# Performance work log

Measured on AMD Instinct MI355X. Metric: run time of the kernel, lower is better.

The kernel has to match this reference:

```python
import jax, jax.numpy as jnp
import numpy as np

N_HEAD = 32
N_KV_HEAD = 8
HEAD_DIM = 64
ROPE_BASE = 10000.0


def _rope_cos_sin(T, dtype):
    # inv_freq over even dims; freqs: [T, HEAD_DIM//2]
    inv_freq = 1.0 / (ROPE_BASE ** (jnp.arange(0, HEAD_DIM, 2, dtype=jnp.float32) / HEAD_DIM))
    freqs = jnp.arange(T, dtype=jnp.float32)[:, None] * inv_freq[None, :]
    return jnp.cos(freqs).astype(dtype), jnp.sin(freqs).astype(dtype)


def _apply_rope(x, cos, sin):
    # x: [B, H, T, D]; cos/sin: [T, D//2]. Original chunks cat(freqs,freqs) so
    # cos1==cos2==cos(freqs), sin1==sin2==sin(freqs) -> standard rotate-half.
    x1, x2 = jnp.split(x, 2, axis=-1)
    c = cos[None, None]
    s = sin[None, None]
    return jnp.concatenate([x1 * c - x2 * s, x1 * s + x2 * c], axis=-1)


def setup_inputs() -> dict:
    key = jax.random.key(0)
    ks = jax.random.split(key, 5)
    B, T, C = 2, 2048, 2048
    kv_dim = N_KV_HEAD * HEAD_DIM
    sc = 1.0 / np.sqrt(C)
    return {
        "x": jax.random.normal(ks[0], (B, T, C), jnp.float32),
        "Wq": jax.random.normal(ks[1], (C, C), jnp.float32) * sc,
        "Wk": jax.random.normal(ks[2], (C, kv_dim), jnp.float32) * sc,
        "Wv": jax.random.normal(ks[3], (C, kv_dim), jnp.float32) * sc,
        "Wo": jax.random.normal(ks[4], (C, C), jnp.float32) * sc,
    }


def reference(x, Wq, Wk, Wv, Wo):
    B, T, C = x.shape
    n_rep = N_HEAD // N_KV_HEAD
    # projections -> [B, H, T, D]
    q = (x @ Wq).reshape(B, T, N_HEAD, HEAD_DIM).transpose(0, 2, 1, 3)
    k = (x @ Wk).reshape(B, T, N_KV_HEAD, HEAD_DIM).transpose(0, 2, 1, 3)
    v = (x @ Wv).reshape(B, T, N_KV_HEAD, HEAD_DIM).transpose(0, 2, 1, 3)
    cos, sin = _rope_cos_sin(T, x.dtype)
    q = _apply_rope(q, cos, sin)
    k = _apply_rope(k, cos, sin)
    # GQA: q head h attends kv head h // n_rep (repeat_interleave semantics).
    # Group q as [B, KV, n_rep, T, D] and broadcast k/v instead of materializing.
    qg = q.reshape(B, N_KV_HEAD, n_rep, T, HEAD_DIM)
    scale = 1.0 / np.sqrt(HEAD_DIM)
    scores = jnp.einsum("bgrqd,bgkd->bgrqk", qg, k) * scale  # [B,KV,rep,T,T]
    causal = jnp.tril(jnp.ones((T, T), dtype=bool))
    scores = jnp.where(causal[None, None, None], scores, -jnp.inf)
    att = jax.nn.softmax(scores, axis=-1)
    y = jnp.einsum("bgrqk,bgkd->bgrqd", att, v)  # [B,KV,rep,T,D]
    y = y.reshape(B, N_HEAD, T, HEAD_DIM).transpose(0, 2, 1, 3).reshape(B, T, C)
    return y @ Wo
```

## Files before the change

kernel.cpp:

```cpp
#include <hip/hip_runtime.h>
#include <hip/hip_bf16.h>


typedef __hip_bfloat16 bf16_t;
typedef __bf16 bf16x8 __attribute__((ext_vector_type(8)));
typedef float f32x4 __attribute__((ext_vector_type(4)));

#define AS1 __attribute__((address_space(1)))
#define AS3 __attribute__((address_space(3)))

__device__ __forceinline__ void gload_lds16(const void* g, void* l) {
  __builtin_amdgcn_global_load_lds((const AS1 unsigned int*)g,
                                   (AS3 unsigned int*)l, 16, 0, 0);
}

__device__ __forceinline__ float fast_exp2(float x) {
#if __has_builtin(__builtin_amdgcn_exp2f)
  return __builtin_amdgcn_exp2f(x);
#else
  return exp2f(x);
#endif
}

__device__ __forceinline__ unsigned int pack_bf16_rnd(unsigned int u0, unsigned int u1) {
  u0 += 0x8000u; u1 += 0x8000u;
#if __has_builtin(__builtin_amdgcn_perm)
  return __builtin_amdgcn_perm(u1, u0, 0x07060302u);
#else
  return (u1 & 0xffff0000u) | (u0 >> 16);
#endif
}

__device__ __forceinline__ void store_out(float* p, float v) { *p = v; }
__device__ __forceinline__ void store_out(bf16_t* p, float v) { *p = __float2bfloat16(v); }

__global__ void cast_f32_bf16(const float* __restrict__ src, bf16_t* __restrict__ dst, int n4) {
  int i = blockIdx.x * blockDim.x + threadIdx.x;
  if (i >= n4) return;
  float4 v = ((const float4*)src)[i];
  bf16_t o[4] = {__float2bfloat16(v.x), __float2bfloat16(v.y),
                 __float2bfloat16(v.z), __float2bfloat16(v.w)};
  ((ushort4*)dst)[i] = *(ushort4*)o;
}

__global__ void wtrans_cast(const float* __restrict__ W, bf16_t* __restrict__ dst, int ncols) {
  __shared__ float tile[32][33];
  int tx = threadIdx.x, ty = threadIdx.y;
  int n0 = blockIdx.x * 32, k0 = blockIdx.y * 32;
#pragma unroll
  for (int i = 0; i < 4; ++i)
    tile[ty + 8 * i][tx] = W[(long)(k0 + ty + 8 * i) * ncols + n0 + tx];
  __syncthreads();
#pragma unroll
  for (int i = 0; i < 4; ++i)
    dst[(long)(n0 + ty + 8 * i) * 2048 + k0 + tx] = __float2bfloat16(tile[tx][ty + 8 * i]);
}

__global__ void rope_kernel(bf16_t* __restrict__ qkv) {
  int i = blockIdx.x * 256 + threadIdx.x;
  int oct = i & 3;
  int rem = i >> 2;
  int hp = rem % 40;
  int row = rem / 40;
  int t = row & 2047;
  int colbase = (hp < 32) ? (hp * 64) : (2048 + (hp - 32) * 64);
  long base = (long)row * 3072 + colbase + oct * 8;
  bf16x8 x1 = *(bf16x8*)(qkv + base);
  bf16x8 x2 = *(bf16x8*)(qkv + base + 32);
  float sc = (hp < 32) ? 0.18033688011112043f : 1.0f;
  bf16x8 o1, o2;
#pragma unroll
  for (int jj = 0; jj < 8; ++jj) {
    int d = oct * 8 + jj;
    float inv_freq = exp2f(-(float)d * 0.4152410118074032f);
    float ang = (float)t * inv_freq;
    float sv, cv;
    sincosf(ang, &sv, &cv);
    float a = __bfloat162float(((const __hip_bfloat16*)&x1)[jj]);
    float b = __bfloat162float(((const __hip_bfloat16*)&x2)[jj]);
    ((__hip_bfloat16*)&o1)[jj] = __float2bfloat16((a * cv - b * sv) * sc);
    ((__hip_bfloat16*)&o2)[jj] = __float2bfloat16((a * sv + b * cv) * sc);
  }
  *(bf16x8*)(qkv + base) = o1;
  *(bf16x8*)(qkv + base + 32) = o2;
}

__global__ void transpose_v(const bf16_t* __restrict__ qkv, bf16_t* __restrict__ vt) {
  __shared__ bf16_t tile[32][33];
  int tx = threadIdx.x, ty = threadIdx.y;
  int t0 = blockIdx.x * 32, d0 = blockIdx.y * 32, bk = blockIdx.z;
  int bb = bk >> 3, kv = bk & 7;
  const bf16_t* src = qkv + (long)(bb * 2048) * 3072 + 2560 + kv * 64;
#pragma unroll
  for (int i = 0; i < 4; ++i)
    tile[ty + 8 * i][tx] = src[(long)(t0 + ty + 8 * i) * 3072 + d0 + tx];
  __syncthreads();
#pragma unroll
  for (int i = 0; i < 4; ++i)
    vt[((long)bk * 64 + d0 + ty + 8 * i) * 2048 + t0 + tx] = tile[tx][ty + 8 * i];
}

template <typename OutT>
__global__ __launch_bounds__(256, 2)
void gemm_bt(const bf16_t* __restrict__ A, const bf16_t* __restrict__ Bt,
             OutT* __restrict__ C, int M, int N, int K) {
  __shared__ __align__(16) bf16_t As[128 * 64];
  __shared__ __align__(16) bf16_t Bs[128 * 64];
  const int tid = threadIdx.x;
  const int wave = tid >> 6, lane = tid & 63, g = lane >> 4, l15 = lane & 15;
  const int m0 = blockIdx.y * 128, n0 = blockIdx.x * 128;
  const int mw = (wave >> 1) * 64, nw = (wave & 1) * 64;
  const bf16_t* Ab = A + (long)m0 * K;
  const bf16_t* Bb = Bt + (long)n0 * K;
  f32x4 acc[4][4] = {};
  const int nkt = K >> 6;
  for (int kt = 0; kt < nkt; ++kt) {
    __syncthreads();
#pragma unroll
    for (int i = 0; i < 4; ++i) {
      int c = i * 256 + tid;
      int row = c >> 3, pos = c & 7;
      int gcol = ((pos ^ (row & 7)) * 8);
      gload_lds16(Ab + (long)row * K + kt * 64 + gcol, &As[c * 8]);
      gload_lds16(Bb + (long)row * K + kt * 64 + gcol, &Bs[c * 8]);
    }
    __syncthreads();
#pragma unroll
    for (int ks = 0; ks < 2; ++ks) {
      bf16x8 af[4], bq[4];
#pragma unroll
      for (int i = 0; i < 4; ++i) {
        int pos = ((ks * 4 + g) ^ (l15 & 7)) * 8;
        af[i] = *(const bf16x8*)&As[(mw + i * 16 + l15) * 64 + pos];
        bq[i] = *(const bf16x8*)&Bs[(nw + i * 16 + l15) * 64 + pos];
      }
#pragma unroll
      for (int i = 0; i < 4; ++i)
#pragma unroll
        for (int j = 0; j < 4; ++j)
          acc[i][j] = __builtin_amdgcn_mfma_f32_16x16x32_bf16(af[i], bq[j], acc[i][j], 0, 0, 0);
    }
  }
#pragma unroll
  for (int i = 0; i < 4; ++i)
#pragma unroll
    for (int j = 0; j < 4; ++j) {
      int r = m0 + mw + i * 16 + g * 4;
      int cn = n0 + nw + j * 16 + l15;
#pragma unroll
      for (int ii = 0; ii < 4; ++ii)
        store_out(&C[(long)(r + ii) * N + cn], acc[i][j][ii]);
    }
}

__global__ __launch_bounds__(256, 2)
void flash_attn(const bf16_t* __restrict__ qkv, const bf16_t* __restrict__ vt,
                bf16_t* __restrict__ y) {
  constexpr int T = 2048, LDQ = 3072;
  __shared__ __align__(16) bf16_t Ks[2][128 * 64];
  __shared__ __align__(16) bf16_t Vs[2][64 * 128];
  __shared__ __align__(16) bf16_t Ps[4][1280];
  const int tid = threadIdx.x, wave = tid >> 6, lane = tid & 63, g = lane >> 4, l15 = lane & 15;
  const int qt = gridDim.x - 1 - blockIdx.x;
  const int h = blockIdx.y, b = blockIdx.z;
  const int kvh = h >> 2;
  const bf16_t* qbase = qkv + (long)(b * T + qt * 128) * LDQ + h * 64;
  const bf16_t* kbase = qkv + (long)(b * T) * LDQ + 2048 + kvh * 64;
  const bf16_t* vbase = vt + (long)((b * 8 + kvh) * 64) * T;

  bf16x8 qf[2][2];
#pragma unroll
  for (int ms = 0; ms < 2; ++ms)
#pragma unroll
    for (int hh = 0; hh < 2; ++hh)
      qf[ms][hh] = *(const bf16x8*)(qbase + (long)(wave * 32 + ms * 16 + l15) * LDQ + hh * 32 + g * 8);

  bf16x8 onef;
#pragma unroll
  for (int i = 0; i < 8; ++i) onef[i] = (__bf16)1.0f;

  f32x4 o[2][4] = {};
  f32x4 lacc[2] = {};
  bf16_t* Pw = &Ps[wave][0];
  const int sw = (l15 >> 1) & 3;
  const f32x4 fz = {0.f, 0.f, 0.f, 0.f};

  auto stage = [&](int kt, int buf) {
#pragma unroll
    for (int i = 0; i < 4; ++i) {
      int c = i * 256 + tid;
      { int row = c >> 3, pos = c & 7;
        gload_lds16(kbase + (long)(kt * 128 + row) * LDQ + ((pos ^ (row & 7)) * 8),
                    &Ks[buf][c * 8]); }
      { int row = c >> 4, pos = c & 15;
        gload_lds16(vbase + (long)row * T + kt * 128 + ((pos ^ (row & 15)) * 8),
                    &Vs[buf][c * 8]); }
    }
  };

  stage(0, 0);
  const int nkt = qt + 1;
  for (int kt = 0; kt < nkt; ++kt) {
    __syncthreads();
    if (kt < qt) stage(kt + 1, (kt + 1) & 1);
    const bf16_t* Kc = Ks[kt & 1];
    const bf16_t* Vc = Vs[kt & 1];
    const bool diag = (kt == qt);

#pragma unroll
    for (int ks = 0; ks < 4; ++ks) {
      f32x4 s[2][2];
#pragma unroll
      for (int nsl = 0; nsl < 2; ++nsl) {
        int krow = ks * 32 + nsl * 16 + l15;
        bf16x8 kf0 = *(const bf16x8*)&Kc[krow * 64 + ((g ^ (l15 & 7)) * 8)];
        bf16x8 kf1 = *(const bf16x8*)&Kc[krow * 64 + (((4 + g) ^ (l15 & 7)) * 8)];
#pragma unroll
        for (int ms = 0; ms < 2; ++ms) {
          f32x4 t = __builtin_amdgcn_mfma_f32_16x16x32_bf16(kf0, qf[ms][0], fz, 0, 0, 0);
          s[ms][nsl] = __builtin_amdgcn_mfma_f32_16x16x32_bf16(kf1, qf[ms][1], t, 0, 0, 0);
        }
      }
      bf16x8 pf[2];
#pragma unroll
      for (int ms = 0; ms < 2; ++ms) {
#pragma unroll
        for (int nsl = 0; nsl < 2; ++nsl) {
          unsigned int u[4];
#pragma unroll
          for (int ii = 0; ii < 4; ++ii) {
            float p = fast_exp2(s[ms][nsl][ii]);
            if (diag && (ks * 32 + nsl * 16 + g * 4 + ii > wave * 32 + ms * 16 + l15)) p = 0.f;
            u[ii] = __builtin_bit_cast(unsigned int, p);
          }
          uint2 dw;
          dw.x = pack_bf16_rnd(u[0], u[1]);
          dw.y = pack_bf16_rnd(u[2], u[3]);
          int pp = (nsl * 2 + (g >> 1)) ^ sw;
          *(uint2*)&Pw[(ms * 16 + l15) * 32 + pp * 8 + (g & 1) * 4] = dw;
        }
        pf[ms] = *(const bf16x8*)&Pw[(ms * 16 + l15) * 32 + ((g ^ sw) * 8)];
        lacc[ms] = __builtin_amdgcn_mfma_f32_16x16x32_bf16(pf[ms], onef, lacc[ms], 0, 0, 0);
      }
#pragma unroll
      for (int ds = 0; ds < 4; ++ds) {
        bf16x8 vf = *(const bf16x8*)&Vc[(ds * 16 + l15) * 128 + (((ks * 4 + g) ^ l15) * 8)];
        o[0][ds] = __builtin_amdgcn_mfma_f32_16x16x32_bf16(pf[0], vf, o[0][ds], 0, 0, 0);
        o[1][ds] = __builtin_amdgcn_mfma_f32_16x16x32_bf16(pf[1], vf, o[1][ds], 0, 0, 0);
      }
    }
  }

  bf16_t* E = &Ps[wave][0];
#pragma unroll
  for (int ms = 0; ms < 2; ++ms) {
    f32x4 linv;
#pragma unroll
    for (int ii = 0; ii < 4; ++ii) linv[ii] = 1.0f / lacc[ms][ii];
#pragma unroll
    for (int ds = 0; ds < 4; ++ds)
#pragma unroll
      for (int ii = 0; ii < 4; ++ii)
        E[(g * 4 + ii) * 72 + ds * 16 + l15] = __float2bfloat16(o[ms][ds][ii] * linv[ii]);
    bf16x8 r0 = *(const bf16x8*)&E[l15 * 72 + g * 16];
    bf16x8 r1 = *(const bf16x8*)&E[l15 * 72 + g * 16 + 8];
    int q = qt * 128 + wave * 32 + ms * 16 + l15;
    *(bf16x8*)&y[(long)(b * T + q) * 2048 + h * 64 + g * 16] = r0;
    *(bf16x8*)&y[(long)(b * T + q) * 2048 + h * 64 + g * 16 + 8] = r1;
  }
}

extern "C" void kernel_launch(void* const* d_in, const int* in_sizes, int n_in,
                              void* d_out, int out_size, void* d_ws, size_t ws_size,
                              hipStream_t stream) {
  const float* x  = (const float*)d_in[0];
  const float* Wq = (const float*)d_in[1];
  const float* Wk = (const float*)d_in[2];
  const float* Wv = (const float*)d_in[3];
  const float* Wo = (const float*)d_in[4];
  float* out = (float*)d_out;
  char* ws = (char*)d_ws;

  bf16_t* xb    = (bf16_t*)(ws);
  bf16_t* wqkvt = (bf16_t*)(ws + 16777216);
  bf16_t* wot   = (bf16_t*)(ws + 16777216 + 12582912);
  bf16_t* qkvb  = (bf16_t*)(ws + 16777216 + 12582912 + 8388608);
  bf16_t* vtb   = (bf16_t*)(ws + 16777216 + 12582912 + 8388608 + 25165824);
  bf16_t* yb = xb;

  dim3 b32(32, 8);
  cast_f32_bf16<<<8192, 256, 0, stream>>>(x, xb, 2097152);
  wtrans_cast<<<dim3(64, 64), b32, 0, stream>>>(Wq, wqkvt, 2048);
  wtrans_cast<<<dim3(16, 64), b32, 0, stream>>>(Wk, wqkvt + 2048L * 2048, 512);
  wtrans_cast<<<dim3(16, 64), b32, 0, stream>>>(Wv, wqkvt + 2560L * 2048, 512);
  wtrans_cast<<<dim3(64, 64), b32, 0, stream>>>(Wo, wot, 2048);
  gemm_bt<bf16_t><<<dim3(24, 32), 256, 0, stream>>>(xb, wqkvt, qkvb, 4096, 3072, 2048);
  rope_kernel<<<2560, 256, 0, stream>>>(qkvb);
  transpose_v<<<dim3(64, 2, 16), b32, 0, stream>>>(qkvb, vtb);
  flash_attn<<<dim3(16, 32, 2), 256, 0, stream>>>(qkvb, vtb, yb);
  gemm_bt<float><<<dim3(16, 32), 256, 0, stream>>>(yb, wot, out, 4096, 2048, 2048);
}
```

Before: 313.7 us.

## Fuse prep and RoPE/V-transpose launches, shrink attention KV tile, raise occupancy

Merges the x cast and all four weight transpose-casts into one launch, and merges RoPE with the V transpose into one launch. This cuts kernel launches and the tail gaps between them. RoPE now uses a manual range reduction with fast __sinf/__cosf instead of sincosf, which gives up some accuracy. Flash attention switches to 64-key tiles to halve LDS use, raises its launch bound to 4 blocks per SM, interleaves heavy and light causal query tiles, and reuses the V buffer for the epilogue. The GEMM launch bound also goes from 2 to 3, which may cause register spills.

```diff
diff --git a/kernel.cpp b/kernel.cpp
--- a/kernel.cpp
+++ b/kernel.cpp
@@ -34,19 +34,30 @@
 __device__ __forceinline__ void store_out(float* p, float v) { *p = v; }
 __device__ __forceinline__ void store_out(bf16_t* p, float v) { *p = __float2bfloat16(v); }
 
-__global__ void cast_f32_bf16(const float* __restrict__ src, bf16_t* __restrict__ dst, int n4) {
-  int i = blockIdx.x * blockDim.x + threadIdx.x;
-  if (i >= n4) return;
-  float4 v = ((const float4*)src)[i];
-  bf16_t o[4] = {__float2bfloat16(v.x), __float2bfloat16(v.y),
-                 __float2bfloat16(v.z), __float2bfloat16(v.w)};
-  ((ushort4*)dst)[i] = *(ushort4*)o;
-}
-
-__global__ void wtrans_cast(const float* __restrict__ W, bf16_t* __restrict__ dst, int ncols) {
+__global__ void prep(const float* __restrict__ x, const float* __restrict__ Wq,
+                     const float* __restrict__ Wk, const float* __restrict__ Wv,
+                     const float* __restrict__ Wo, bf16_t* __restrict__ xb,
+                     bf16_t* __restrict__ wqkvt, bf16_t* __restrict__ wot) {
+  const int bid = blockIdx.x, tid = threadIdx.x;
+  if (bid < 2048) {
+#pragma unroll
+    for (int k = 0; k < 4; ++k) {
+      int i = bid * 1024 + k * 256 + tid;
+      float4 v = ((const float4*)x)[i];
+      bf16_t o[4] = {__float2bfloat16(v.x), __float2bfloat16(v.y),
+                     __float2bfloat16(v.z), __float2bfloat16(v.w)};
+      ((ushort4*)xb)[i] = *(ushort4*)o;
+    }
+    return;
+  }
+  const float* W; bf16_t* dst; int ncols, bx, by;
+  if (bid < 6144)       { int l = bid - 2048;  W = Wq; dst = wqkvt;               ncols = 2048; bx = l & 63; by = l >> 6; }
+  else if (bid < 10240) { int l = bid - 6144;  W = Wo; dst = wot;                 ncols = 2048; bx = l & 63; by = l >> 6; }
+  else if (bid < 11264) { int l = bid - 10240; W = Wk; dst = wqkvt + 2048L * 2048; ncols = 512; bx = l & 15; by = l >> 4; }
+  else                  { int l = bid - 11264; W = Wv; dst = wqkvt + 2560L * 2048; ncols = 512; bx = l & 15; by = l >> 4; }
   __shared__ float tile[32][33];
-  int tx = threadIdx.x, ty = threadIdx.y;
-  int n0 = blockIdx.x * 32, k0 = blockIdx.y * 32;
+  const int tx = tid & 31, ty = tid >> 5;
+  const int n0 = bx * 32, k0 = by * 32;
 #pragma unroll
   for (int i = 0; i < 4; ++i)
     tile[ty + 8 * i][tx] = W[(long)(k0 + ty + 8 * i) * ncols + n0 + tx];
@@ -56,40 +67,46 @@
     dst[(long)(n0 + ty + 8 * i) * 2048 + k0 + tx] = __float2bfloat16(tile[tx][ty + 8 * i]);
 }
 
-__global__ void rope_kernel(bf16_t* __restrict__ qkv) {
-  int i = blockIdx.x * 256 + threadIdx.x;
-  int oct = i & 3;
-  int rem = i >> 2;
-  int hp = rem % 40;
-  int row = rem / 40;
-  int t = row & 2047;
-  int colbase = (hp < 32) ? (hp * 64) : (2048 + (hp - 32) * 64);
-  long base = (long)row * 3072 + colbase + oct * 8;
-  bf16x8 x1 = *(bf16x8*)(qkv + base);
-  bf16x8 x2 = *(bf16x8*)(qkv + base + 32);
-  float sc = (hp < 32) ? 0.18033688011112043f : 1.0f;
-  bf16x8 o1, o2;
-#pragma unroll
-  for (int jj = 0; jj < 8; ++jj) {
-    int d = oct * 8 + jj;
-    float inv_freq = exp2f(-(float)d * 0.4152410118074032f);
-    float ang = (float)t * inv_freq;
-    float sv, cv;
-    sincosf(ang, &sv, &cv);
-    float a = __bfloat162float(((const __hip_bfloat16*)&x1)[jj]);
-    float b = __bfloat162float(((const __hip_bfloat16*)&x2)[jj]);
-    ((__hip_bfloat16*)&o1)[jj] = __float2bfloat16((a * cv - b * sv) * sc);
-    ((__hip_bfloat16*)&o2)[jj] = __float2bfloat16((a * sv + b * cv) * sc);
-  }
-  *(bf16x8*)(qkv + base) = o1;
-  *(bf16x8*)(qkv + base + 32) = o2;
-}
-
-__global__ void transpose_v(const bf16_t* __restrict__ qkv, bf16_t* __restrict__ vt) {
+__global__ void rope_vt(bf16_t* __restrict__ qkv, bf16_t* __restrict__ vt) {
+  const int bid = blockIdx.x, tid = threadIdx.x;
   __shared__ bf16_t tile[32][33];
-  int tx = threadIdx.x, ty = threadIdx.y;
-  int t0 = blockIdx.x * 32, d0 = blockIdx.y * 32, bk = blockIdx.z;
+  if (bid < 2560) {
+    int i = bid * 256 + tid;
+    int oct = i & 3;
+    int rem = i >> 2;
+    int hp = rem % 40;
+    int row = rem / 40;
+    int t = row & 2047;
+    int colbase = (hp < 32) ? (hp * 64) : (2048 + (hp - 32) * 64);
+    long base = (long)row * 3072 + colbase + oct * 8;
+    bf16x8 x1 = *(bf16x8*)(qkv + base);
+    bf16x8 x2 = *(bf16x8*)(qkv + base + 32);
+    float sc = (hp < 32) ? 0.18033688011112043f : 1.0f;
+    bf16x8 o1, o2;
+#pragma unroll
+    for (int jj = 0; jj < 8; ++jj) {
+      int d = oct * 8 + jj;
+      float inv_freq = exp2f(-(float)d * 0.4152410118074032f);
+      float ang = (float)t * inv_freq;
+      float rev = ang * 0.15915494309189535f;
+      float fr = (rev - rintf(rev)) * 6.283185307179586f;
+      float sv = __sinf(fr), cv = __cosf(fr);
+      float a = __bfloat162float(((const __hip_bfloat16*)&x1)[jj]);
+      float b = __bfloat162float(((const __hip_bfloat16*)&x2)[jj]);
+      ((__hip_bfloat16*)&o1)[jj] = __float2bfloat16((a * cv - b * sv) * sc);
+      ((__hip_bfloat16*)&o2)[jj] = __float2bfloat16((a * sv + b * cv) * sc);
+    }
+    *(bf16x8*)(qkv + base) = o1;
+    *(bf16x8*)(qkv + base + 32) = o2;
+    return;
+  }
+  int l = bid - 2560;
+  int t0 = (l & 63) * 32;
+  int rest = l >> 6;
+  int d0 = (rest & 1) * 32;
+  int bk = rest >> 1;
   int bb = bk >> 3, kv = bk & 7;
+  const int tx = tid & 31, ty = tid >> 5;
   const bf16_t* src = qkv + (long)(bb * 2048) * 3072 + 2560 + kv * 64;
 #pragma unroll
   for (int i = 0; i < 4; ++i)
@@ -101,7 +118,7 @@
 }
 
 template <typename OutT>
-__global__ __launch_bounds__(256, 2)
+__global__ __launch_bounds__(256, 3)
 void gemm_bt(const bf16_t* __restrict__ A, const bf16_t* __restrict__ Bt,
              OutT* __restrict__ C, int M, int N, int K) {
   __shared__ __align__(16) bf16_t As[128 * 64];
@@ -153,15 +170,16 @@
     }
 }
 
-__global__ __launch_bounds__(256, 2)
+__global__ __launch_bounds__(256, 4)
 void flash_attn(const bf16_t* __restrict__ qkv, const bf16_t* __restrict__ vt,
                 bf16_t* __restrict__ y) {
   constexpr int T = 2048, LDQ = 3072;
-  __shared__ __align__(16) bf16_t Ks[2][128 * 64];
-  __shared__ __align__(16) bf16_t Vs[2][64 * 128];
-  __shared__ __align__(16) bf16_t Ps[4][1280];
+  __shared__ __align__(16) bf16_t Ks[2][64 * 64];
+  __shared__ __align__(16) bf16_t Vs[2][64 * 64];
+  __shared__ __align__(16) bf16_t Ps[4][1024];
   const int tid = threadIdx.x, wave = tid >> 6, lane = tid & 63, g = lane >> 4, l15 = lane & 15;
-  const int qt = gridDim.x - 1 - blockIdx.x;
+  const int j = blockIdx.x;
+  const int qt = (j < 8) ? (15 - j) : (j - 8);
   const int h = blockIdx.y, b = blockIdx.z;
   const int kvh = h >> 2;
   const bf16_t* qbase = qkv + (long)(b * T + qt * 128) * LDQ + h * 64;
@@ -187,28 +205,28 @@
 
   auto stage = [&](int kt, int buf) {
 #pragma unroll
-    for (int i = 0; i < 4; ++i) {
+    for (int i = 0; i < 2; ++i) {
       int c = i * 256 + tid;
-      { int row = c >> 3, pos = c & 7;
-        gload_lds16(kbase + (long)(kt * 128 + row) * LDQ + ((pos ^ (row & 7)) * 8),
-                    &Ks[buf][c * 8]); }
-      { int row = c >> 4, pos = c & 15;
-        gload_lds16(vbase + (long)row * T + kt * 128 + ((pos ^ (row & 15)) * 8),
-                    &Vs[buf][c * 8]); }
+      int row = c >> 3, pos = c & 7;
+      gload_lds16(kbase + (long)(kt * 64 + row) * LDQ + ((pos ^ (row & 7)) * 8),
+                  &Ks[buf][c * 8]);
+      gload_lds16(vbase + (long)row * T + kt * 64 + ((pos ^ (row & 7)) * 8),
+                  &Vs[buf][c * 8]);
     }
   };
 
   stage(0, 0);
-  const int nkt = qt + 1;
+  const int nkt = 2 * qt + 2;
   for (int kt = 0; kt < nkt; ++kt) {
     __syncthreads();
-    if (kt < qt) stage(kt + 1, (kt + 1) & 1);
+    if (kt + 1 < nkt) stage(kt + 1, (kt + 1) & 1);
     const bf16_t* Kc = Ks[kt & 1];
     const bf16_t* Vc = Vs[kt & 1];
-    const bool diag = (kt == qt);
-
-#pragma unroll
-    for (int ks = 0; ks < 4; ++ks) {
+    const int dk = kt - 2 * qt;
+    const bool diag = (dk >= 0);
+
+#pragma unroll
+    for (int ks = 0; ks < 2; ++ks) {
       f32x4 s[2][2];
 #pragma unroll
       for (int nsl = 0; nsl < 2; ++nsl) {
@@ -230,7 +248,8 @@
 #pragma unroll
           for (int ii = 0; ii < 4; ++ii) {
             float p = fast_exp2(s[ms][nsl][ii]);
-            if (diag && (ks * 32 + nsl * 16 + g * 4 + ii > wave * 32 + ms * 16 + l15)) p = 0.f;
+            if (diag && (dk * 64 + ks * 32 + nsl * 16 + g * 4 + ii >
+                         wave * 32 + ms * 16 + l15)) p = 0.f;
             u[ii] = __builtin_bit_cast(unsigned int, p);
           }
           uint2 dw;
@@ -244,14 +263,15 @@
       }
 #pragma unroll
       for (int ds = 0; ds < 4; ++ds) {
-        bf16x8 vf = *(const bf16x8*)&Vc[(ds * 16 + l15) * 128 + (((ks * 4 + g) ^ l15) * 8)];
+        bf16x8 vf = *(const bf16x8*)&Vc[(ds * 16 + l15) * 64 + (((ks * 4 + g) ^ (l15 & 7)) * 8)];
         o[0][ds] = __builtin_amdgcn_mfma_f32_16x16x32_bf16(pf[0], vf, o[0][ds], 0, 0, 0);
         o[1][ds] = __builtin_amdgcn_mfma_f32_16x16x32_bf16(pf[1], vf, o[1][ds], 0, 0, 0);
       }
     }
   }
 
-  bf16_t* E = &Ps[wave][0];
+  __syncthreads();
+  bf16_t* E = (bf16_t*)&Vs[0][0] + wave * 1152;
 #pragma unroll
   for (int ms = 0; ms < 2; ++ms) {
     f32x4 linv;
@@ -288,15 +308,9 @@
   bf16_t* vtb   = (bf16_t*)(ws + 16777216 + 12582912 + 8388608 + 25165824);
   bf16_t* yb = xb;
 
-  dim3 b32(32, 8);
-  cast_f32_bf16<<<8192, 256, 0, stream>>>(x, xb, 2097152);
-  wtrans_cast<<<dim3(64, 64), b32, 0, stream>>>(Wq, wqkvt, 2048);
-  wtrans_cast<<<dim3(16, 64), b32, 0, stream>>>(Wk, wqkvt + 2048L * 2048, 512);
-  wtrans_cast<<<dim3(16, 64), b32, 0, stream>>>(Wv, wqkvt + 2560L * 2048, 512);
-  wtrans_cast<<<dim3(64, 64), b32, 0, stream>>>(Wo, wot, 2048);
+  prep<<<12288, 256, 0, stream>>>(x, Wq, Wk, Wv, Wo, xb, wqkvt, wot);
   gemm_bt<bf16_t><<<dim3(24, 32), 256, 0, stream>>>(xb, wqkvt, qkvb, 4096, 3072, 2048);
-  rope_kernel<<<2560, 256, 0, stream>>>(qkvb);
-  transpose_v<<<dim3(64, 2, 16), b32, 0, stream>>>(qkvb, vtb);
+  rope_vt<<<4608, 256, 0, stream>>>(qkvb, vtb);
   flash_attn<<<dim3(16, 32, 2), 256, 0, stream>>>(qkvb, vtb, yb);
   gemm_bt<float><<<dim3(16, 32), 256, 0, stream>>>(yb, wot, out, 4096, 2048, 2048);
 }
```

Result: no change. 311.3 us (-0.8%).
